# Kernel tuning notes

Hardware: AMD Instinct MI355X
Metric: run time of the kernel (lower is better)

Reference implementation:

```python
import jax, jax.numpy as jnp
import numpy as np

N_NODES = 100000
N_EDGES = 1600000
F_IN = 128
HID = 128
N_CLS = 10
BN_EPS = 1e-5


def setup_inputs() -> dict:
    key = jax.random.key(0)
    ks = jax.random.split(key, 20)
    d = {}
    d['x'] = jax.random.normal(ks[0], (N_NODES, F_IN), dtype=jnp.float32)
    d['edge_index'] = jax.random.randint(ks[1], (2, N_EDGES), 0, N_NODES, dtype=jnp.int64)
    d['edge_weights'] = jax.random.uniform(ks[2], (N_EDGES,), dtype=jnp.float32)
    s1 = 1.0 / np.sqrt(F_IN)
    s2 = 1.0 / np.sqrt(HID)
    d['W1'] = jax.random.normal(ks[3], (F_IN, HID), dtype=jnp.float32) * s1
    d['b1'] = jax.random.normal(ks[4], (HID,), dtype=jnp.float32) * 0.01
    d['g1'] = jax.random.uniform(ks[5], (HID,), dtype=jnp.float32) + 0.5
    d['be1'] = jax.random.normal(ks[6], (HID,), dtype=jnp.float32) * 0.01
    d['W2'] = jax.random.normal(ks[7], (HID, HID), dtype=jnp.float32) * s2
    d['b2'] = jax.random.normal(ks[8], (HID,), dtype=jnp.float32) * 0.01
    d['g2'] = jax.random.uniform(ks[9], (HID,), dtype=jnp.float32) + 0.5
    d['be2'] = jax.random.normal(ks[10], (HID,), dtype=jnp.float32) * 0.01
    d['W3'] = jax.random.normal(ks[11], (HID, HID), dtype=jnp.float32) * s2
    d['b3'] = jax.random.normal(ks[12], (HID,), dtype=jnp.float32) * 0.01
    d['g3'] = jax.random.uniform(ks[13], (HID,), dtype=jnp.float32) + 0.5
    d['be3'] = jax.random.normal(ks[14], (HID,), dtype=jnp.float32) * 0.01
    d['Wlin'] = jax.random.normal(ks[15], (3 * HID, N_CLS), dtype=jnp.float32) / np.sqrt(3 * HID)
    d['blin'] = jax.random.normal(ks[16], (N_CLS,), dtype=jnp.float32) * 0.01
    return d


def _gcn_norm(edge_index, edge_weights, n):
    # add self loops with weight 1 (PyG gcn_norm default fill_value=1)
    loops = jnp.arange(n, dtype=edge_index.dtype)
    row = jnp.concatenate([edge_index[0], loops])   # source j
    col = jnp.concatenate([edge_index[1], loops])   # target i
    ew = jnp.concatenate([edge_weights, jnp.ones((n,), edge_weights.dtype)])
    deg = jax.ops.segment_sum(ew, col, num_segments=n)  # in-degree by weight
    dis = jnp.where(deg > 0, jax.lax.rsqrt(deg), 0.0)
    norm = dis[row] * ew * dis[col]                     # [E+N]
    return row, col, norm


def _gcn_conv(x, row, col, norm, W, b, n):
    h = x @ W                                            # [N, H]
    msg = h[row] * norm[:, None]                         # gather + scale
    out = jax.ops.segment_sum(msg, col, num_segments=n)  # scatter-add
    return out + b


def _bn_relu(x, g, be):
    # BatchNorm with track_running_stats=False: batch stats, biased variance
    mean = jnp.mean(x, axis=0)
    var = jnp.mean((x - mean) ** 2, axis=0)
    y = (x - mean) * jax.lax.rsqrt(var + BN_EPS) * g + be
    return jax.nn.relu(y)


def reference(x, edge_index, edge_weights, W1, b1, g1, be1, W2, b2, g2, be2,
              W3, b3, g3, be3, Wlin, blin):
    n = x.shape[0]
    row, col, norm = _gcn_norm(edge_index, edge_weights, n)
    o1 = _bn_relu(_gcn_conv(x, row, col, norm, W1, b1, n), g1, be1)
    o2 = _bn_relu(_gcn_conv(o1, row, col, norm, W2, b2, n), g2, be2)
    o3 = _bn_relu(_gcn_conv(o2, row, col, norm, W3, b3, n), g3, be3)
    emb = jnp.concatenate([o1, o2, o3], axis=1)          # [N, 3H]
    return emb @ Wlin + blin                             # [N, C]
```

## Files before the change

kernel.cpp:

```cpp
#include <hip/hip_runtime.h>

#define BN_EPS 1e-5f
#define AGG_GRID 2048
#define NB 512
#define CAP 4864
#define BIN_KE 16

typedef __attribute__((ext_vector_type(8))) short short8;
typedef __attribute__((ext_vector_type(4))) float f32x4;

static __device__ __forceinline__ float4 ld4(const float* p){ return *reinterpret_cast<const float4*>(p); }
static __device__ __forceinline__ unsigned short f2bf(float f){
  unsigned u = __float_as_uint(f);
  u += 0x7fffu + ((u>>16)&1u);
  return (unsigned short)(u>>16);
}
static __device__ __forceinline__ void fma_bf4(float4& a, float s, uint2 w){
  float v0 = __uint_as_float(w.x << 16);
  float v1 = __uint_as_float(w.x & 0xffff0000u);
  float v2 = __uint_as_float(w.y << 16);
  float v3 = __uint_as_float(w.y & 0xffff0000u);
  a.x = fmaf(s,v0,a.x); a.y = fmaf(s,v1,a.y); a.z = fmaf(s,v2,a.z); a.w = fmaf(s,v3,a.w);
}
static __device__ __forceinline__ float4 unpack_bf4(uint2 w){
  return make_float4(__uint_as_float(w.x << 16), __uint_as_float(w.x & 0xffff0000u),
                     __uint_as_float(w.y << 16), __uint_as_float(w.y & 0xffff0000u));
}
static __device__ __forceinline__ uint2 pack_bf4(float4 v){
  uint2 pk;
  pk.x = (unsigned)f2bf(v.x) | ((unsigned)f2bf(v.y)<<16);
  pk.y = (unsigned)f2bf(v.z) | ((unsigned)f2bf(v.w)<<16);
  return pk;
}

__global__ __launch_bounds__(256) void k_prep(const float* __restrict__ W0, const float* __restrict__ W1,
                                              const float* __restrict__ W2, const float* __restrict__ Wlin,
                                              unsigned short* __restrict__ Wt, unsigned short* __restrict__ WlinT,
                                              int* __restrict__ bucketCnt, float* __restrict__ red64){
  int idx = blockIdx.x*256 + threadIdx.x;
  if (idx < NB) bucketCnt[idx] = 0;
  int widx = idx - 1024;
  if (widx >= 0 && widx < 49152){
    int l = widx >> 14, rem = widx & 16383;
    int k = rem >> 7, n = rem & 127;
    const float* W = (l==0) ? W0 : ((l==1) ? W1 : W2);
    Wt[(size_t)l*16384 + n*128 + k] = f2bf(W[rem]);
  }
  int lidx = widx - 49152;
  if (lidx >= 0 && lidx < 6144){
    int l = lidx >> 11, rem = lidx & 2047;
    int n = rem >> 7, k = rem & 127;
    float v = (n < 10) ? Wlin[((size_t)l*128 + k)*10 + n] : 0.f;
    WlinT[(size_t)l*2048 + n*128 + k] = f2bf(v);
  }
  int ridx = lidx - 6144;
  if (ridx >= 0 && ridx < 49152) red64[ridx] = 0.f;
}

__global__ __launch_bounds__(256) void k_bin(const int* __restrict__ row, const int* __restrict__ col,
                                             const float* __restrict__ ew, int* __restrict__ bucketCnt,
                                             int2* __restrict__ bin, int E){
  __shared__ int hist[NB];
  int t = threadIdx.x;
  hist[t] = 0; hist[t+256] = 0;
  __syncthreads();
  int base0 = blockIdx.x*(256*BIN_KE) + t;
  int rank[BIN_KE];
  #pragma unroll
  for (int j=0;j<BIN_KE;++j){
    int e = base0 + j*256;
    if (e < E) rank[j] = atomicAdd(&hist[col[e]>>8], 1);
  }
  __syncthreads();
  int c0 = hist[t], c1 = hist[t+256];
  __syncthreads();
  if (c0) hist[t]     = atomicAdd(&bucketCnt[t],     c0);
  if (c1) hist[t+256] = atomicAdd(&bucketCnt[t+256], c1);
  __syncthreads();
  #pragma unroll
  for (int j=0;j<BIN_KE;++j){
    int e = base0 + j*256;
    if (e < E){
      int d = col[e];
      int bk = d >> 8;
      int pos = hist[bk] + rank[j];
      if (pos < CAP)
        bin[(size_t)bk*CAP + pos] = make_int2(row[e] | ((d & 255) << 17), __float_as_int(ew[e]));
    }
  }
}

__global__ __launch_bounds__(256) void k_csr(const int2* __restrict__ bin, const int* __restrict__ bucketCnt,
                                             int2* __restrict__ csr, int* __restrict__ rstart,
                                             float* __restrict__ dis, int N){
  __shared__ int hist[256], scn[256];
  __shared__ float degl[256];
  int b = blockIdx.x, t = threadIdx.x;
  int v = 0;
  if (t < b){ int c = bucketCnt[t]; v = c > CAP ? CAP : c; }
  if (t+256 < b){ int c = bucketCnt[t+256]; v += (c > CAP ? CAP : c); }
  scn[t] = v;
  __syncthreads();
  for (int off=128; off; off>>=1){
    if (t < off) scn[t] += scn[t+off];
    __syncthreads();
  }
  int base = scn[0];
  __syncthreads();
  hist[t] = 0; degl[t] = 0.f;
  __syncthreads();
  int m = bucketCnt[b]; if (m > CAP) m = CAP;
  const int2* bb = bin + (size_t)b*CAP;
  for (int i = t; i < m; i += 256){
    int2 r = bb[i];
    int dl = (r.x >> 17) & 255;
    atomicAdd(&hist[dl], 1);
    atomicAdd(&degl[dl], __int_as_float(r.y));
  }
  __syncthreads();
  int c = hist[t];
  scn[t] = c;
  __syncthreads();
  for (int off=1; off<256; off<<=1){
    int x = (t>=off) ? scn[t-off] : 0;
    __syncthreads();
    scn[t] += x;
    __syncthreads();
  }
  int g = (b<<8) + t;
  if (g < N){
    rstart[g] = base + scn[t] - c;
    dis[g] = rsqrtf(1.f + degl[t]);
    if (g == N-1) rstart[N] = base + scn[t];
  }
  __syncthreads();
  hist[t] = scn[t] - c;
  __syncthreads();
  for (int i = t; i < m; i += 256){
    int2 r = bb[i];
    int dl = (r.x >> 17) & 255;
    int pos = atomicAdd(&hist[dl], 1);
    csr[base + pos] = make_int2(r.x & 0x1FFFF, r.y);
  }
}

template<bool BN, bool LIN, bool LININIT>
__global__ __launch_bounds__(256) void k_gemm_mfma(const void* __restrict__ Ap, const unsigned short* __restrict__ Wt,
                                                   const float* __restrict__ abv, const float* __restrict__ dis,
                                                   unsigned short* __restrict__ h,
                                                   const unsigned short* __restrict__ WlinT,
                                                   const float* __restrict__ blin, float* __restrict__ out, int N){
  __shared__ unsigned short Al[64*136];
  __shared__ unsigned short Wl[128*136];
  int t = threadIdx.x;
  int row0 = blockIdx.x*64;
  #pragma unroll
  for (int i=0;i<8;++i){
    int idx = t + 256*i;
    int r = idx>>5, cg = idx&31;
    float4 v;
    if (!BN){
      v = make_float4(0.f,0.f,0.f,0.f);
      if (row0 + r < N) v = ld4((const float*)Ap + ((size_t)(row0+r)<<7) + cg*4);
    } else {
      uint2 raw = make_uint2(0u,0u);
      if (row0 + r < N) raw = *reinterpret_cast<const uint2*>((const unsigned short*)Ap + ((size_t)(row0+r)<<7) + cg*4);
      v = unpack_bf4(raw);
      float4 av = ld4(abv + cg*4), cv = ld4(abv + 128 + cg*4);
      v.x = fmaxf(fmaf(v.x,av.x,cv.x),0.f);
      v.y = fmaxf(fmaf(v.y,av.y,cv.y),0.f);
      v.z = fmaxf(fmaf(v.z,av.z,cv.z),0.f);
      v.w = fmaxf(fmaf(v.w,av.w,cv.w),0.f);
    }
    *reinterpret_cast<uint2*>(&Al[r*136 + cg*4]) = pack_bf4(v);
  }
  #pragma unroll
  for (int i=0;i<8;++i){
    int idx = t + 256*i;
    int n = idx>>4, c8 = idx&15;
    *reinterpret_cast<uint4*>(&Wl[n*136 + c8*8]) =
      *reinterpret_cast<const uint4*>(&Wt[n*128 + c8*8]);
  }

  int w = t>>6, lane = t&63, quad = lane>>4, lr = lane&15;
  short8 bl[4];
  if (LIN){
    #pragma unroll
    for (int q4=0;q4<4;++q4)
      bl[q4] = *reinterpret_cast<const short8*>(&WlinT[lr*128 + q4*32 + quad*8]);
  }
  __syncthreads();

  f32x4 acc[8];
  #pragma unroll
  for (int j=0;j<8;++j) acc[j] = (f32x4){0.f,0.f,0.f,0.f};
  f32x4 accL = (f32x4){0.f,0.f,0.f,0.f};
  #pragma unroll
  for (int kk=0; kk<128; kk+=32){
    short8 a = *reinterpret_cast<const short8*>(&Al[(w*16+lr)*136 + kk + quad*8]);
    #pragma unroll
    for (int j=0;j<8;++j){
      short8 b = *reinterpret_cast<const short8*>(&Wl[(j*16+lr)*136 + kk + quad*8]);
      acc[j] = __builtin_amdgcn_mfma_f32_16x16x32_bf16(a, b, acc[j], 0, 0, 0);
    }
    if (LIN) accL = __builtin_amdgcn_mfma_f32_16x16x32_bf16(a, bl[kk>>5], accL, 0, 0, 0);
  }
  if (LIN && lr < 10){
    #pragma unroll
    for (int r=0;r<4;++r){
      int rr = row0 + w*16 + quad*4 + r;
      if (rr < N){
        if (LININIT) out[(size_t)rr*10 + lr] = blin[lr] + accL[r];
        else         out[(size_t)rr*10 + lr] += accL[r];
      }
    }
  }
  float drow[4];
  #pragma unroll
  for (int r=0;r<4;++r){
    int rr = row0 + w*16 + quad*4 + r;
    drow[r] = (rr < N) ? dis[rr] : 0.f;
  }
  __syncthreads();
  #pragma unroll
  for (int j=0;j<8;++j)
    #pragma unroll
    for (int r=0;r<4;++r)
      Al[(w*16 + quad*4 + r)*136 + j*16 + lr] = f2bf(acc[j][r] * drow[r]);
  __syncthreads();
  #pragma unroll
  for (int i=0;i<8;++i){
    int idx = t + 256*i;
    int r = idx>>5, cg = idx&31;
    if (row0 + r < N)
      *reinterpret_cast<uint2*>(&h[((size_t)(row0+r)<<7) + cg*4]) =
        *reinterpret_cast<const uint2*>(&Al[r*136 + cg*4]);
  }
}

__global__ __launch_bounds__(256) void k_agg(const unsigned short* __restrict__ h, const int2* __restrict__ csr,
                                             const int* __restrict__ rstart, const float* __restrict__ dis,
                                             const float* __restrict__ bias, unsigned short* __restrict__ o,
                                             float* __restrict__ red64, int N){
  __shared__ float ls[256];
  int t = threadIdx.x;
  ls[t] = 0.f;
  __syncthreads();
  int lane = t & 31, gy = t >> 5;
  float4 bv = ld4(bias + lane*4);
  float4 ssum = make_float4(0.f,0.f,0.f,0.f);
  float4 ssq  = make_float4(0.f,0.f,0.f,0.f);
  for (int g = blockIdx.x*8 + gy; g < N; g += AGG_GRID*8){
    int s = rstart[g], n = rstart[g+1] - s;
    float dg = dis[g];
    float4 acc = unpack_bf4(*reinterpret_cast<const uint2*>(h + ((size_t)g<<7) + lane*4));
    int i = 0;
    for (; i+3 < n; i += 4){
      int2 e0 = csr[s+i], e1 = csr[s+i+1], e2 = csr[s+i+2], e3 = csr[s+i+3];
      uint2 r0 = *reinterpret_cast<const uint2*>(h + ((size_t)e0.x<<7) + lane*4);
      uint2 r1 = *reinterpret_cast<const uint2*>(h + ((size_t)e1.x<<7) + lane*4);
      uint2 r2 = *reinterpret_cast<const uint2*>(h + ((size_t)e2.x<<7) + lane*4);
      uint2 r3 = *reinterpret_cast<const uint2*>(h + ((size_t)e3.x<<7) + lane*4);
      fma_bf4(acc, __int_as_float(e0.y), r0);
      fma_bf4(acc, __int_as_float(e1.y), r1);
      fma_bf4(acc, __int_as_float(e2.y), r2);
      fma_bf4(acc, __int_as_float(e3.y), r3);
    }
    for (; i < n; ++i){
      int2 e0 = csr[s+i];
      fma_bf4(acc, __int_as_float(e0.y), *reinterpret_cast<const uint2*>(h + ((size_t)e0.x<<7) + lane*4));
    }
    acc.x = fmaf(acc.x, dg, bv.x); acc.y = fmaf(acc.y, dg, bv.y);
    acc.z = fmaf(acc.z, dg, bv.z); acc.w = fmaf(acc.w, dg, bv.w);
    *reinterpret_cast<uint2*>(o + ((size_t)g<<7) + lane*4) = pack_bf4(acc);
    ssum.x += acc.x; ssum.y += acc.y; ssum.z += acc.z; ssum.w += acc.w;
    ssq.x = fmaf(acc.x,acc.x,ssq.x); ssq.y = fmaf(acc.y,acc.y,ssq.y);
    ssq.z = fmaf(acc.z,acc.z,ssq.z); ssq.w = fmaf(acc.w,acc.w,ssq.w);
  }
  int f = lane*4;
  atomicAdd(&ls[f+0], ssum.x); atomicAdd(&ls[f+1], ssum.y);
  atomicAdd(&ls[f+2], ssum.z); atomicAdd(&ls[f+3], ssum.w);
  atomicAdd(&ls[128+f+0], ssq.x); atomicAdd(&ls[128+f+1], ssq.y);
  atomicAdd(&ls[128+f+2], ssq.z); atomicAdd(&ls[128+f+3], ssq.w);
  __syncthreads();
  atomicAdd(&red64[(size_t)(blockIdx.x & 63)*256 + t], ls[t]);
}

__global__ void k_bn_fin(const float* __restrict__ red64, const float* __restrict__ gam,
                         const float* __restrict__ bet, float* __restrict__ ab, int N){
  __shared__ float sh[256];
  int t = threadIdx.x;
  float s = 0.f;
  #pragma unroll 4
  for (int i=0;i<64;++i) s += red64[(size_t)i*256 + t];
  sh[t] = s;
  __syncthreads();
  if (t < 128){
    float invN = 1.f/(float)N;
    float mean = sh[t]*invN;
    float var = fmaxf(sh[128+t]*invN - mean*mean, 0.f);
    float a = gam[t]*rsqrtf(var + BN_EPS);
    ab[t] = a;
    ab[128+t] = bet[t] - mean*a;
  }
}

__global__ __launch_bounds__(256) void k_lin(const unsigned short* __restrict__ o, const float* __restrict__ Wl_g,
                                             const float* __restrict__ ab, float* __restrict__ out, int N){
  __shared__ float Wl[1280];
  __shared__ float abL[256];
  int t = threadIdx.x;
  for (int i=t;i<1280;i+=256) Wl[i] = Wl_g[i];
  abL[t] = ab[t];
  __syncthreads();
  int row = blockIdx.x*256 + t;
  if (row >= N) return;
  float acc[10];
  #pragma unroll
  for (int c=0;c<10;++c) acc[c] = out[(size_t)row*10 + c];
  const unsigned short* orow = o + ((size_t)row<<7);
  #pragma unroll 4
  for (int k=0;k<128;k+=4){
    float4 v = unpack_bf4(*reinterpret_cast<const uint2*>(orow + k));
    float4 av = ld4(abL + k), cv = ld4(abL + 128 + k);
    v.x = fmaxf(fmaf(v.x,av.x,cv.x),0.f);
    v.y = fmaxf(fmaf(v.y,av.y,cv.y),0.f);
    v.z = fmaxf(fmaf(v.z,av.z,cv.z),0.f);
    v.w = fmaxf(fmaf(v.w,av.w,cv.w),0.f);
    #pragma unroll
    for (int c=0;c<10;++c){
      acc[c] = fmaf(v.x, Wl[(k+0)*10+c], acc[c]);
      acc[c] = fmaf(v.y, Wl[(k+1)*10+c], acc[c]);
      acc[c] = fmaf(v.z, Wl[(k+2)*10+c], acc[c]);
      acc[c] = fmaf(v.w, Wl[(k+3)*10+c], acc[c]);
    }
  }
  #pragma unroll
  for (int c=0;c<10;++c) out[(size_t)row*10 + c] = acc[c];
}


extern "C" void kernel_launch(void* const* d_in, const int* in_sizes, int n_in,
                              void* d_out, int out_size, void* d_ws, size_t ws_size,
                              hipStream_t stream){
  const float* x    = (const float*)d_in[0];
  const int*   ei   = (const int*)d_in[1];
  const float* ew   = (const float*)d_in[2];
  const float* W[3]  = {(const float*)d_in[3], (const float*)d_in[7],  (const float*)d_in[11]};
  const float* b[3]  = {(const float*)d_in[4], (const float*)d_in[8],  (const float*)d_in[12]};
  const float* g[3]  = {(const float*)d_in[5], (const float*)d_in[9],  (const float*)d_in[13]};
  const float* be[3] = {(const float*)d_in[6], (const float*)d_in[10], (const float*)d_in[14]};
  const float* Wlin = (const float*)d_in[15];
  const float* blin = (const float*)d_in[16];
  float* out = (float*)d_out;

  int N = in_sizes[0] / 128;
  int E = in_sizes[2];
  const int* row = ei;
  const int* col = ei + E;

  char* p = (char*)d_ws;
  auto carve = [&](size_t bytes) -> void* {
    void* q = (void*)p;
    p += (bytes + 255) & ~(size_t)255;
    return q;
  };
  int*   bucketCnt = (int*)  carve((size_t)NB*4);
  float* dis      = (float*)carve((size_t)N*4);
  int*   rstart   = (int*)  carve((size_t)(N+1)*4);
  float* red64    = (float*)carve((size_t)3*64*256*4);
  float* ab       = (float*)carve(3*256*4);
  unsigned short* Wt    = (unsigned short*)carve((size_t)3*128*128*2);
  unsigned short* WlinT = (unsigned short*)carve((size_t)3*16*128*2);
  unsigned short* h  = (unsigned short*)carve((size_t)N*128*2);
  unsigned short* o  = (unsigned short*)carve((size_t)N*128*2);
  int2*  csr      = (int2*) carve((size_t)E*8);
  int2*  bin      = (int2*) carve((size_t)NB*CAP*8);

  int gN = (N+255)/256;
  int gBin = (E + 256*BIN_KE - 1) / (256*BIN_KE);

  k_prep<<<412,256,0,stream>>>(W[0], W[1], W[2], Wlin, Wt, WlinT, bucketCnt, red64);
  k_bin <<<gBin,256,0,stream>>>(row, col, ew, bucketCnt, bin, E);
  k_csr <<<NB,256,0,stream>>>(bin, bucketCnt, csr, rstart, dis, N);

  int gGemm = (N+63)/64;
  k_gemm_mfma<false,false,false><<<gGemm,256,0,stream>>>(x, Wt, nullptr, dis, h, nullptr, nullptr, nullptr, N);
  k_agg   <<<AGG_GRID,256,0,stream>>>(h, csr, rstart, dis, b[0], o, red64, N);
  k_bn_fin<<<1,256,0,stream>>>(red64, g[0], be[0], ab, N);
  k_gemm_mfma<true,true,true><<<gGemm,256,0,stream>>>(o, Wt + 16384, ab, dis, h, WlinT, blin, out, N);
  k_agg   <<<AGG_GRID,256,0,stream>>>(h, csr, rstart, dis, b[1], o, red64 + 16384, N);
  k_bn_fin<<<1,256,0,stream>>>(red64 + 16384, g[1], be[1], ab + 256, N);
  k_gemm_mfma<true,true,false><<<gGemm,256,0,stream>>>(o, Wt + 32768, ab + 256, dis, h, WlinT + 2048, blin, out, N);
  k_agg   <<<AGG_GRID,256,0,stream>>>(h, csr, rstart, dis, b[2], o, red64 + 32768, N);
  k_bn_fin<<<1,256,0,stream>>>(red64 + 32768, g[2], be[2], ab + 512, N);
  k_lin<<<gN,256,0,stream>>>(o, Wlin + (size_t)2*1280, ab + 512, out, N);
}
```

Measured before the change: 487.0 us.

## Slice features into 8 column blocks and pack CSR edges into 32 bits

Stores h and o as 8 feature slices of 16 columns each, so every aggregation block handles one slice. A slice of all nodes is 3.2MB, small enough to stay cache-resident during the random gather. CSR entries are packed into 32 bits (17-bit source index plus 15-bit quantized weight), which halves the edge-stream traffic. The cost is that each edge list is now read 8 times, once per slice, and the edge weights lose precision to 15-bit quantization.

```diff
diff --git a/kernel.cpp b/kernel.cpp
--- a/kernel.cpp
+++ b/kernel.cpp
@@ -15,13 +15,6 @@
   u += 0x7fffu + ((u>>16)&1u);
   return (unsigned short)(u>>16);
 }
-static __device__ __forceinline__ void fma_bf4(float4& a, float s, uint2 w){
-  float v0 = __uint_as_float(w.x << 16);
-  float v1 = __uint_as_float(w.x & 0xffff0000u);
-  float v2 = __uint_as_float(w.y << 16);
-  float v3 = __uint_as_float(w.y & 0xffff0000u);
-  a.x = fmaf(s,v0,a.x); a.y = fmaf(s,v1,a.y); a.z = fmaf(s,v2,a.z); a.w = fmaf(s,v3,a.w);
-}
 static __device__ __forceinline__ float4 unpack_bf4(uint2 w){
   return make_float4(__uint_as_float(w.x << 16), __uint_as_float(w.x & 0xffff0000u),
                      __uint_as_float(w.y << 16), __uint_as_float(w.y & 0xffff0000u));
@@ -31,6 +24,12 @@
   pk.x = (unsigned)f2bf(v.x) | ((unsigned)f2bf(v.y)<<16);
   pk.y = (unsigned)f2bf(v.z) | ((unsigned)f2bf(v.w)<<16);
   return pk;
+}
+static __device__ __forceinline__ float2 unpack_bf2(unsigned w){
+  return make_float2(__uint_as_float(w << 16), __uint_as_float(w & 0xffff0000u));
+}
+static __device__ __forceinline__ unsigned pack_bf2(float2 v){
+  return (unsigned)f2bf(v.x) | ((unsigned)f2bf(v.y)<<16);
 }
 
 __global__ __launch_bounds__(256) void k_prep(const float* __restrict__ W0, const float* __restrict__ W1,
@@ -91,7 +90,7 @@
 }
 
 __global__ __launch_bounds__(256) void k_csr(const int2* __restrict__ bin, const int* __restrict__ bucketCnt,
-                                             int2* __restrict__ csr, int* __restrict__ rstart,
+                                             unsigned* __restrict__ csr, int* __restrict__ rstart,
                                              float* __restrict__ dis, int N){
   __shared__ int hist[256], scn[256];
   __shared__ float degl[256];
@@ -140,7 +139,9 @@
     int2 r = bb[i];
     int dl = (r.x >> 17) & 255;
     int pos = atomicAdd(&hist[dl], 1);
-    csr[base + pos] = make_int2(r.x & 0x1FFFF, r.y);
+    int eq = (int)(__int_as_float(r.y) * 32768.0f);
+    if (eq > 32767) eq = 32767;
+    csr[base + pos] = (unsigned)(r.x & 0x1FFFF) | ((unsigned)eq << 17);
   }
 }
 
@@ -154,25 +155,33 @@
   __shared__ unsigned short Wl[128*136];
   int t = threadIdx.x;
   int row0 = blockIdx.x*64;
-  #pragma unroll
-  for (int i=0;i<8;++i){
-    int idx = t + 256*i;
-    int r = idx>>5, cg = idx&31;
-    float4 v;
-    if (!BN){
-      v = make_float4(0.f,0.f,0.f,0.f);
+  if (!BN){
+    #pragma unroll
+    for (int i=0;i<8;++i){
+      int idx = t + 256*i;
+      int r = idx>>5, cg = idx&31;
+      float4 v = make_float4(0.f,0.f,0.f,0.f);
       if (row0 + r < N) v = ld4((const float*)Ap + ((size_t)(row0+r)<<7) + cg*4);
-    } else {
+      *reinterpret_cast<uint2*>(&Al[r*136 + cg*4]) = pack_bf4(v);
+    }
+  } else {
+    const unsigned short* o = (const unsigned short*)Ap;
+    #pragma unroll
+    for (int i=0;i<8;++i){
+      int idx = t + 256*i;
+      int s = idx >> 8, rem = idx & 255;
+      int r = rem >> 2, sub = rem & 3;
       uint2 raw = make_uint2(0u,0u);
-      if (row0 + r < N) raw = *reinterpret_cast<const uint2*>((const unsigned short*)Ap + ((size_t)(row0+r)<<7) + cg*4);
-      v = unpack_bf4(raw);
-      float4 av = ld4(abv + cg*4), cv = ld4(abv + 128 + cg*4);
+      if (row0 + r < N) raw = *reinterpret_cast<const uint2*>(&o[((size_t)s*N + row0 + r)*16 + sub*4]);
+      float4 v = unpack_bf4(raw);
+      int f0 = s*16 + sub*4;
+      float4 av = ld4(abv + f0), cv = ld4(abv + 128 + f0);
       v.x = fmaxf(fmaf(v.x,av.x,cv.x),0.f);
       v.y = fmaxf(fmaf(v.y,av.y,cv.y),0.f);
       v.z = fmaxf(fmaf(v.z,av.z,cv.z),0.f);
       v.w = fmaxf(fmaf(v.w,av.w,cv.w),0.f);
-    }
-    *reinterpret_cast<uint2*>(&Al[r*136 + cg*4]) = pack_bf4(v);
+      *reinterpret_cast<uint2*>(&Al[r*136 + f0]) = pack_bf4(v);
+    }
   }
   #pragma unroll
   for (int i=0;i<8;++i){
@@ -231,59 +240,66 @@
   #pragma unroll
   for (int i=0;i<8;++i){
     int idx = t + 256*i;
-    int r = idx>>5, cg = idx&31;
+    int s = idx >> 8, rem = idx & 255;
+    int r = rem >> 2, sub = rem & 3;
     if (row0 + r < N)
-      *reinterpret_cast<uint2*>(&h[((size_t)(row0+r)<<7) + cg*4]) =
-        *reinterpret_cast<const uint2*>(&Al[r*136 + cg*4]);
-  }
-}
-
-__global__ __launch_bounds__(256) void k_agg(const unsigned short* __restrict__ h, const int2* __restrict__ csr,
+      *reinterpret_cast<uint2*>(&h[((size_t)s*N + row0 + r)*16 + sub*4]) =
+        *reinterpret_cast<const uint2*>(&Al[r*136 + s*16 + sub*4]);
+  }
+}
+
+__global__ __launch_bounds__(256) void k_agg(const unsigned short* __restrict__ h, const unsigned* __restrict__ csr,
                                              const int* __restrict__ rstart, const float* __restrict__ dis,
                                              const float* __restrict__ bias, unsigned short* __restrict__ o,
                                              float* __restrict__ red64, int N){
-  __shared__ float ls[256];
+  __shared__ float ls[32];
   int t = threadIdx.x;
-  ls[t] = 0.f;
-  __syncthreads();
-  int lane = t & 31, gy = t >> 5;
-  float4 bv = ld4(bias + lane*4);
-  float4 ssum = make_float4(0.f,0.f,0.f,0.f);
-  float4 ssq  = make_float4(0.f,0.f,0.f,0.f);
-  for (int g = blockIdx.x*8 + gy; g < N; g += AGG_GRID*8){
-    int s = rstart[g], n = rstart[g+1] - s;
+  int s = blockIdx.x & 7, group = blockIdx.x >> 3;
+  int lane8 = t & 7, slot = t >> 3;
+  if (t < 32) ls[t] = 0.f;
+  __syncthreads();
+  const unsigned short* hs = h + (size_t)s*N*16;
+  unsigned short* os = o + (size_t)s*N*16;
+  float2 bv = make_float2(bias[s*16 + lane8*2], bias[s*16 + lane8*2 + 1]);
+  float2 ssum = make_float2(0.f,0.f), ssq = make_float2(0.f,0.f);
+  const float qs = 1.f/32768.f;
+  for (int g = group*32 + slot; g < N; g += (AGG_GRID/8)*32){
+    int st = rstart[g], n = rstart[g+1] - st;
     float dg = dis[g];
-    float4 acc = unpack_bf4(*reinterpret_cast<const uint2*>(h + ((size_t)g<<7) + lane*4));
+    float2 acc = unpack_bf2(*reinterpret_cast<const unsigned*>(&hs[(size_t)g*16 + lane8*2]));
     int i = 0;
     for (; i+3 < n; i += 4){
-      int2 e0 = csr[s+i], e1 = csr[s+i+1], e2 = csr[s+i+2], e3 = csr[s+i+3];
-      uint2 r0 = *reinterpret_cast<const uint2*>(h + ((size_t)e0.x<<7) + lane*4);
-      uint2 r1 = *reinterpret_cast<const uint2*>(h + ((size_t)e1.x<<7) + lane*4);
-      uint2 r2 = *reinterpret_cast<const uint2*>(h + ((size_t)e2.x<<7) + lane*4);
-      uint2 r3 = *reinterpret_cast<const uint2*>(h + ((size_t)e3.x<<7) + lane*4);
-      fma_bf4(acc, __int_as_float(e0.y), r0);
-      fma_bf4(acc, __int_as_float(e1.y), r1);
-      fma_bf4(acc, __int_as_float(e2.y), r2);
-      fma_bf4(acc, __int_as_float(e3.y), r3);
+      unsigned e0 = csr[st+i], e1 = csr[st+i+1], e2 = csr[st+i+2], e3 = csr[st+i+3];
+      unsigned r0 = *reinterpret_cast<const unsigned*>(&hs[(size_t)(e0 & 0x1FFFF)*16 + lane8*2]);
+      unsigned r1 = *reinterpret_cast<const unsigned*>(&hs[(size_t)(e1 & 0x1FFFF)*16 + lane8*2]);
+      unsigned r2 = *reinterpret_cast<const unsigned*>(&hs[(size_t)(e2 & 0x1FFFF)*16 + lane8*2]);
+      unsigned r3 = *reinterpret_cast<const unsigned*>(&hs[(size_t)(e3 & 0x1FFFF)*16 + lane8*2]);
+      float w0 = (float)(e0 >> 17) * qs, w1 = (float)(e1 >> 17) * qs;
+      float w2 = (float)(e2 >> 17) * qs, w3 = (float)(e3 >> 17) * qs;
+      float2 v0 = unpack_bf2(r0), v1 = unpack_bf2(r1), v2 = unpack_bf2(r2), v3 = unpack_bf2(r3);
+      acc.x = fmaf(w0, v0.x, acc.x); acc.y = fmaf(w0, v0.y, acc.y);
+      acc.x = fmaf(w1, v1.x, acc.x); acc.y = fmaf(w1, v1.y, acc.y);
+      acc.x = fmaf(w2, v2.x, acc.x); acc.y = fmaf(w2, v2.y, acc.y);
+      acc.x = fmaf(w3, v3.x, acc.x); acc.y = fmaf(w3, v3.y, acc.y);
     }
     for (; i < n; ++i){
-      int2 e0 = csr[s+i];
-      fma_bf4(acc, __int_as_float(e0.y), *reinterpret_cast<const uint2*>(h + ((size_t)e0.x<<7) + lane*4));
-    }
-    acc.x = fmaf(acc.x, dg, bv.x); acc.y = fmaf(acc.y, dg, bv.y);
-    acc.z = fmaf(acc.z, dg, bv.z); acc.w = fmaf(acc.w, dg, bv.w);
-    *reinterpret_cast<uint2*>(o + ((size_t)g<<7) + lane*4) = pack_bf4(acc);
-    ssum.x += acc.x; ssum.y += acc.y; ssum.z += acc.z; ssum.w += acc.w;
+      unsigned e0 = csr[st+i];
+      unsigned r0 = *reinterpret_cast<const unsigned*>(&hs[(size_t)(e0 & 0x1FFFF)*16 + lane8*2]);
+      float w0 = (float)(e0 >> 17) * qs;
+      float2 v0 = unpack_bf2(r0);
+      acc.x = fmaf(w0, v0.x, acc.x); acc.y = fmaf(w0, v0.y, acc.y);
+    }
+    acc.x = fmaf(acc.x, dg, bv.x);
+    acc.y = fmaf(acc.y, dg, bv.y);
+    *reinterpret_cast<unsigned*>(&os[(size_t)g*16 + lane8*2]) = pack_bf2(acc);
+    ssum.x += acc.x; ssum.y += acc.y;
     ssq.x = fmaf(acc.x,acc.x,ssq.x); ssq.y = fmaf(acc.y,acc.y,ssq.y);
-    ssq.z = fmaf(acc.z,acc.z,ssq.z); ssq.w = fmaf(acc.w,acc.w,ssq.w);
-  }
-  int f = lane*4;
-  atomicAdd(&ls[f+0], ssum.x); atomicAdd(&ls[f+1], ssum.y);
-  atomicAdd(&ls[f+2], ssum.z); atomicAdd(&ls[f+3], ssum.w);
-  atomicAdd(&ls[128+f+0], ssq.x); atomicAdd(&ls[128+f+1], ssq.y);
-  atomicAdd(&ls[128+f+2], ssq.z); atomicAdd(&ls[128+f+3], ssq.w);
-  __syncthreads();
-  atomicAdd(&red64[(size_t)(blockIdx.x & 63)*256 + t], ls[t]);
+  }
+  atomicAdd(&ls[lane8*2],      ssum.x); atomicAdd(&ls[lane8*2+1],      ssum.y);
+  atomicAdd(&ls[16+lane8*2],   ssq.x);  atomicAdd(&ls[16+lane8*2+1],   ssq.y);
+  __syncthreads();
+  if (t < 16)       atomicAdd(&red64[(size_t)(group & 63)*256 + s*16 + t], ls[t]);
+  else if (t < 32)  atomicAdd(&red64[(size_t)(group & 63)*256 + 128 + s*16 + (t-16)], ls[t]);
 }
 
 __global__ void k_bn_fin(const float* __restrict__ red64, const float* __restrict__ gam,
@@ -318,21 +334,25 @@
   float acc[10];
   #pragma unroll
   for (int c=0;c<10;++c) acc[c] = out[(size_t)row*10 + c];
-  const unsigned short* orow = o + ((size_t)row<<7);
-  #pragma unroll 4
-  for (int k=0;k<128;k+=4){
-    float4 v = unpack_bf4(*reinterpret_cast<const uint2*>(orow + k));
-    float4 av = ld4(abL + k), cv = ld4(abL + 128 + k);
-    v.x = fmaxf(fmaf(v.x,av.x,cv.x),0.f);
-    v.y = fmaxf(fmaf(v.y,av.y,cv.y),0.f);
-    v.z = fmaxf(fmaf(v.z,av.z,cv.z),0.f);
-    v.w = fmaxf(fmaf(v.w,av.w,cv.w),0.f);
-    #pragma unroll
-    for (int c=0;c<10;++c){
-      acc[c] = fmaf(v.x, Wl[(k+0)*10+c], acc[c]);
-      acc[c] = fmaf(v.y, Wl[(k+1)*10+c], acc[c]);
-      acc[c] = fmaf(v.z, Wl[(k+2)*10+c], acc[c]);
-      acc[c] = fmaf(v.w, Wl[(k+3)*10+c], acc[c]);
+  #pragma unroll
+  for (int s8=0; s8<8; ++s8){
+    const unsigned short* op = o + ((size_t)s8*N + row)*16;
+    #pragma unroll
+    for (int sub=0; sub<4; ++sub){
+      float4 v = unpack_bf4(*reinterpret_cast<const uint2*>(op + sub*4));
+      int k = s8*16 + sub*4;
+      float4 av = ld4(abL + k), cv = ld4(abL + 128 + k);
+      v.x = fmaxf(fmaf(v.x,av.x,cv.x),0.f);
+      v.y = fmaxf(fmaf(v.y,av.y,cv.y),0.f);
+      v.z = fmaxf(fmaf(v.z,av.z,cv.z),0.f);
+      v.w = fmaxf(fmaf(v.w,av.w,cv.w),0.f);
+      #pragma unroll
+      for (int c=0;c<10;++c){
+        acc[c] = fmaf(v.x, Wl[(k+0)*10+c], acc[c]);
+        acc[c] = fmaf(v.y, Wl[(k+1)*10+c], acc[c]);
+        acc[c] = fmaf(v.z, Wl[(k+2)*10+c], acc[c]);
+        acc[c] = fmaf(v.w, Wl[(k+3)*10+c], acc[c]);
+      }
     }
   }
   #pragma unroll
@@ -374,7 +394,7 @@
   unsigned short* WlinT = (unsigned short*)carve((size_t)3*16*128*2);
   unsigned short* h  = (unsigned short*)carve((size_t)N*128*2);
   unsigned short* o  = (unsigned short*)carve((size_t)N*128*2);
-  int2*  csr      = (int2*) carve((size_t)E*8);
+  unsigned* csr   = (unsigned*)carve((size_t)E*4);
   int2*  bin      = (int2*) carve((size_t)NB*CAP*8);
 
   int gN = (N+255)/256;
```

Measured after the change: 532.3 us. 9.3% more time.
